# Optimization experiments

Hardware: AMD Instinct MI355X
Metric: run time of the kernel (lower is better)

The kernel has to match this reference:

```python
import jax, jax.numpy as jnp
import numpy as np

VOCAB, EMB, H, L, B, S = 100000, 300, 256, 2, 64, 512


def _lstm_cell(x, h, c, w_ih, w_hh, b_ih, b_hh):
    # PyTorch gate order: i, f, g, o
    g = x @ w_ih.T + h @ w_hh.T + (b_ih + b_hh)
    i, f, gg, o = jnp.split(g, 4, axis=-1)
    i, f, o = jax.nn.sigmoid(i), jax.nn.sigmoid(f), jax.nn.sigmoid(o)
    c_new = f * c + i * jnp.tanh(gg)
    h_new = o * jnp.tanh(c_new)
    return h_new, c_new


def setup_inputs() -> dict:
    key = jax.random.key(0)
    ks = jax.random.split(key, 16)
    k = 1.0 / np.sqrt(H)
    u = lambda kk, shape: jax.random.uniform(kk, shape, jnp.float32, -k, k)
    inp = {
        "contexts": jax.random.randint(ks[0], (B, S), 0, VOCAB),
        "positions": jax.random.randint(ks[1], (B,), 0, S),
        "emb": jax.random.normal(ks[2], (VOCAB, EMB), jnp.float32) * 0.1,
        # layer 0: input width EMB; layer 1: input width 2H. dim0 = direction (fwd, bwd)
        "w_ih_l0": u(ks[3], (2, 4 * H, EMB)),
        "w_hh_l0": u(ks[4], (2, 4 * H, H)),
        "b_ih_l0": u(ks[5], (2, 4 * H)),
        "b_hh_l0": u(ks[6], (2, 4 * H)),
        "w_ih_l1": u(ks[7], (2, 4 * H, 2 * H)),
        "w_hh_l1": u(ks[8], (2, 4 * H, H)),
        "b_ih_l1": u(ks[9], (2, 4 * H)),
        "b_hh_l1": u(ks[10], (2, 4 * H)),
        "w_cls": u(ks[11], (2, 2 * H)),
        "b_cls": u(ks[12], (2,)),
    }
    return inp


def reference(emb, w_ih_l0, w_hh_l0, b_ih_l0, b_hh_l0,
              w_ih_l1, w_hh_l1, b_ih_l1, b_hh_l1,
              w_cls, b_cls, contexts, positions):
    layers = [(w_ih_l0, w_hh_l0, b_ih_l0, b_hh_l0),
              (w_ih_l1, w_hh_l1, b_ih_l1, b_hh_l1)]
    bsz = contexts.shape[0]

    def step(carry, tok):
        h, c = carry  # (L, 2, B, H) each
        x = emb[tok]  # (B, EMB) — per-timestep embedding gather
        new_h, new_c = [], []
        for l, (wih, whh, bih, bhh) in enumerate(layers):
            outs = []
            # NOTE: original calls the bidirectional LSTM with seq_len=1 while
            # threading hidden state, so BOTH directions step forward in time.
            for d in range(2):
                hh, cc = _lstm_cell(x, h[l, d], c[l, d], wih[d], whh[d], bih[d], bhh[d])
                outs.append(hh); new_h.append(hh); new_c.append(cc)
            x = jnp.concatenate(outs, axis=-1)  # (B, 2H) -> input to next layer
        h = jnp.stack(new_h).reshape(len(layers), 2, bsz, H)
        c = jnp.stack(new_c).reshape(len(layers), 2, bsz, H)
        return (h, c), x

    h0 = jnp.zeros((len(layers), 2, bsz, H), jnp.float32)
    carry0 = (h0, h0)
    tokens = contexts.T  # (S, B): scan over sequence dim
    _, contexts_encoded = jax.lax.scan(step, carry0, tokens)  # (S, B, 2H)

    # gather encoded state at each item's target position
    target_output = contexts_encoded[positions, jnp.arange(bsz)]  # (B, 2H)
    logits = target_output @ w_cls.T + b_cls  # (B, 2)
    probs = jax.nn.sigmoid(logits)
    return (logits, probs, target_output)
```

## Files before the change

kernel.cpp:

```cpp
#include <hip/hip_runtime.h>
#include <hip/hip_cooperative_groups.h>


typedef short v8s __attribute__((ext_vector_type(8)));
typedef float v4f __attribute__((ext_vector_type(4)));
typedef unsigned long long u64;

#define S_LEN 512
#define BATCH 64
#define EMBD  300
#define XPAD  320
#define ROWP0 584
#define ROWP1 776

__device__ inline unsigned short f2bf(float x) {
  union { float f; unsigned u; } v; v.f = x;
  unsigned r = v.u + 0x7FFF + ((v.u >> 16) & 1);
  return (unsigned short)(r >> 16);
}
__device__ inline float sigm(float x) { return 1.f / (1.f + __expf(-x)); }
__device__ inline float tanhf_(float x) {
  float e = __expf(-2.f * fabsf(x));
  float r = (1.f - e) / (1.f + e);
  return x >= 0.f ? r : -r;
}

__device__ inline v8s ld_sys16(const unsigned short* p) {
  union { u64 q[2]; v8s s; } u;
  u.q[0] = __hip_atomic_load((const u64*)p,     __ATOMIC_RELAXED, __HIP_MEMORY_SCOPE_SYSTEM);
  u.q[1] = __hip_atomic_load((const u64*)p + 1, __ATOMIC_RELAXED, __HIP_MEMORY_SCOPE_SYSTEM);
  return u.s;
}
__device__ inline float ldf_sys(const float* p) {
  return __hip_atomic_load(p, __ATOMIC_RELAXED, __HIP_MEMORY_SCOPE_SYSTEM);
}
__device__ inline void st4_sys(unsigned* p, unsigned v) {
  __hip_atomic_store(p, v, __ATOMIC_RELAXED, __HIP_MEMORY_SCOPE_SYSTEM);
}
__device__ inline void stf_sys(float* p, float v) {
  __hip_atomic_store(p, v, __ATOMIC_RELAXED, __HIP_MEMORY_SCOPE_SYSTEM);
}

__device__ inline void wait_ge(unsigned* c, unsigned thr) {
  while (__hip_atomic_load(c, __ATOMIC_RELAXED, __HIP_MEMORY_SCOPE_AGENT) < thr)
    __builtin_amdgcn_s_sleep(1);
}
__device__ inline void arrive(unsigned* c) {
  __hip_atomic_fetch_add(c, 1u, __ATOMIC_RELAXED, __HIP_MEMORY_SCOPE_AGENT);
}

template<int NK1, int NK2, int P2OFF, bool C1, bool C2>
__device__ inline void step_mm(const unsigned short* __restrict__ aP1,
                               const unsigned short* __restrict__ aP2,
                               const unsigned short* lds_t0,
                               const unsigned short* lds_t1,
                               v4f& acc0, v4f& acc1) {
  v8s a[NK1 + NK2];
#pragma unroll
  for (int i = 0; i < NK1; ++i)
    a[i] = C1 ? ld_sys16(aP1 + i * 32) : *(const v8s*)(aP1 + i * 32);
#pragma unroll
  for (int i = 0; i < NK2; ++i)
    a[NK1 + i] = C2 ? ld_sys16(aP2 + i * 32) : *(const v8s*)(aP2 + i * 32);
#pragma unroll
  for (int i = 0; i < NK1; ++i) {
    v8s b0 = *(const v8s*)(lds_t0 + i * 32);
    v8s b1 = *(const v8s*)(lds_t1 + i * 32);
    acc0 = __builtin_amdgcn_mfma_f32_16x16x32_bf16(a[i], b0, acc0, 0, 0, 0);
    acc1 = __builtin_amdgcn_mfma_f32_16x16x32_bf16(a[i], b1, acc1, 0, 0, 0);
  }
#pragma unroll
  for (int i = 0; i < NK2; ++i) {
    v8s b0 = *(const v8s*)(lds_t0 + P2OFF + i * 32);
    v8s b1 = *(const v8s*)(lds_t1 + P2OFF + i * 32);
    acc0 = __builtin_amdgcn_mfma_f32_16x16x32_bf16(a[NK1 + i], b0, acc0, 0, 0, 0);
    acc1 = __builtin_amdgcn_mfma_f32_16x16x32_bf16(a[NK1 + i], b1, acc1, 0, 0, 0);
  }
}

__global__ void __launch_bounds__(128, 1)
ContextAwareModel_9655086481739_kernel(
    const int* __restrict__ contexts, const int* __restrict__ positions,
    const float* __restrict__ emb,
    const float* __restrict__ wih0, const float* __restrict__ whh0,
    const float* __restrict__ bih0, const float* __restrict__ bhh0,
    const float* __restrict__ wih1, const float* __restrict__ whh1,
    const float* __restrict__ bih1, const float* __restrict__ bhh1,
    const float* __restrict__ wcls, const float* __restrict__ bcls,
    float* __restrict__ out, unsigned char* __restrict__ ws)
{
  __shared__ unsigned short smem[32 * ROWP1];

  const int wg   = blockIdx.x;
  const int tid  = threadIdx.x;
  const int layer  = wg >> 7;
  const int d      = (wg >> 6) & 1;
  const int colblk = (wg >> 1) & 31;
  const int mhalf  = wg & 1;
  const int wv   = tid >> 6;
  const int lane = tid & 63;
  const int quad = lane >> 4;
  const int lc   = lane & 15;
  const int hc0  = colblk * 8;
  const int hc   = hc0 + (lc & 7);
  const int m0   = mhalf * 32 + wv * 16;
  const int r_base = m0 + quad * 4;

  unsigned short* Xbuf  = (unsigned short*)ws;
  unsigned short* h0buf = (unsigned short*)(ws + 20971520u);
  unsigned short* h1buf = (unsigned short*)(ws + 20971520u + 262144u);
  float*          tgt   = (float*)(ws + 20971520u + 262144u + 131072u);
  unsigned*       cnt   = (unsigned*)(ws + 20971520u + 262144u + 131072u + 131072u);

  const int ROWP = layer ? ROWP1 : ROWP0;

  {
    for (int i = wg * 128 + tid; i < 196608; i += 256 * 128) h0buf[i] = 0;
    if (wg == 0) { for (int i = tid; i < 512; i += 128) cnt[i] = 0; }
  }
  {
    int gw2 = wg * 2 + wv;
    for (int rl = 0; rl < 64; ++rl) {
      int rr = gw2 * 64 + rl;
      int t = rr >> 6, b = rr & 63;
      int tok = contexts[b * S_LEN + t];
      const float* erow = emb + (long)tok * EMBD;
#pragma unroll
      for (int i = 0; i < 5; ++i) {
        int kk = i * 64 + lane;
        float v = (kk < EMBD) ? erow[kk] : 0.f;
        if (kk < XPAD) Xbuf[rr * XPAD + kk] = f2bf(v);
      }
    }
  }
  {
    const float* wih = layer ? wih1 : wih0;
    const float* whh = layer ? whh1 : whh0;
    const int KI  = layer ? 512 : 300;
    const int KIp = layer ? 512 : 320;
    const int KT  = layer ? 768 : 576;
    int lr = tid >> 2, sub = tid & 3;
    int c = lr & 15, T = lr >> 4;
    int gate = T * 2 + (c >> 3);
    int j = gate * 256 + hc0 + (c & 7);
    const float* wri = wih + (long)(d * 1024 + j) * KI;
    const float* wrh = whh + (long)(d * 1024 + j) * 256;
    for (int kk = sub; kk < ROWP; kk += 4) {
      float v = 0.f;
      if (kk < KI) v = wri[kk];
      else if (kk >= KIp && kk < KT) v = wrh[kk - KIp];
      smem[lr * ROWP + kk] = f2bf(v);
    }
  }
  float bias0, bias1;
  {
    const float* bi = layer ? bih1 : bih0;
    const float* bh = layer ? bhh1 : bhh0;
    int j0 = ((lc >> 3) & 1) * 256 + hc;
    int j1 = (2 + ((lc >> 3) & 1)) * 256 + hc;
    bias0 = bi[d * 1024 + j0] + bh[d * 1024 + j0];
    bias1 = bi[d * 1024 + j1] + bh[d * 1024 + j1];
  }
  int pos[4];
#pragma unroll
  for (int j = 0; j < 4; ++j) pos[j] = positions[r_base + j];

  float cst[4] = {0.f, 0.f, 0.f, 0.f};

  const unsigned short* lds_t0 = smem + lc * ROWP + quad * 8;
  const unsigned short* lds_t1 = smem + (16 + lc) * ROWP + quad * 8;

  cooperative_groups::grid_group gg = cooperative_groups::this_grid();
  __syncthreads();
  gg.sync();

  const bool hi = (lc & 8) != 0;

  if (layer == 0) {
    unsigned* c_own = cnt + (0 + d * 2 + mhalf) * 64;
    unsigned* c_l1a = cnt + (4 + 0 + mhalf) * 64;
    unsigned* c_l1b = cnt + (4 + 2 + mhalf) * 64;
    for (int t = 0; t < S_LEN; ++t) {
      if (tid == 0) {
        if (t) wait_ge(c_own, 32u * t);
        if (t >= 4) {
          unsigned thr = 32u * (t - 3);
          wait_ge(c_l1a, thr); wait_ge(c_l1b, thr);
        }
      }
      __syncthreads();
      v4f acc0 = {bias0, bias0, bias0, bias0};
      v4f acc1 = {bias1, bias1, bias1, bias1};
      const unsigned short* aP1 = Xbuf + (t * BATCH + m0 + lc) * XPAD + quad * 8;
      const unsigned short* aP2 = h0buf + ((t + 3) & 3) * 32768 + (m0 + lc) * 512 + d * 256 + quad * 8;
      step_mm<10, 8, 320, false, true>(aP1, aP2, lds_t0, lds_t1, acc0, acc1);
#pragma unroll
      for (int j = 0; j < 4; ++j) {
        float a0 = acc0[j], a1 = acc1[j];
        float o0 = __shfl_xor(a0, 8);
        float o1 = __shfl_xor(a1, 8);
        float iv = hi ? o0 : a0;
        float fv = hi ? a0 : o0;
        float gv = hi ? o1 : a1;
        float ov = hi ? a1 : o1;
        float ii = sigm(iv), ff = sigm(fv), ggt = tanhf_(gv), oo = sigm(ov);
        float cn = ff * cst[j] + ii * ggt;
        cst[j] = cn;
        float hv = oo * tanhf_(cn);
        unsigned hb = f2bf(hv);
        unsigned ob = ((unsigned)__shfl_xor((int)hb, 1)) & 0xFFFFu;
        if (lc < 8 && !(lc & 1)) {
          unsigned word = hb | (ob << 16);
          st4_sys((unsigned*)&h0buf[(t & 3) * 32768 + (r_base + j) * 512 + d * 256 + hc], word);
        }
      }
      asm volatile("s_waitcnt vmcnt(0)" ::: "memory");
      __syncthreads();
      if (tid == 0) arrive(c_own);
    }
  } else {
    unsigned* c_own = cnt + (4 + d * 2 + mhalf) * 64;
    unsigned* c_h0a = cnt + (0 + 0 + mhalf) * 64;
    unsigned* c_h0b = cnt + (0 + 2 + mhalf) * 64;
    for (int t = 0; t < S_LEN; ++t) {
      if (tid == 0) {
        unsigned thr = 32u * (t + 1);
        wait_ge(c_h0a, thr); wait_ge(c_h0b, thr);
        if (t) wait_ge(c_own, 32u * t);
      }
      __syncthreads();
      v4f acc0 = {bias0, bias0, bias0, bias0};
      v4f acc1 = {bias1, bias1, bias1, bias1};
      const unsigned short* aP1 = h0buf + (t & 3) * 32768 + (m0 + lc) * 512 + quad * 8;
      const unsigned short* aP2 = h1buf + ((t + 1) & 1) * 32768 + d * 16384 + (m0 + lc) * 256 + quad * 8;
      step_mm<16, 8, 512, true, true>(aP1, aP2, lds_t0, lds_t1, acc0, acc1);
#pragma unroll
      for (int j = 0; j < 4; ++j) {
        float a0 = acc0[j], a1 = acc1[j];
        float o0 = __shfl_xor(a0, 8);
        float o1 = __shfl_xor(a1, 8);
        float iv = hi ? o0 : a0;
        float fv = hi ? a0 : o0;
        float gv = hi ? o1 : a1;
        float ov = hi ? a1 : o1;
        float ii = sigm(iv), ff = sigm(fv), ggt = tanhf_(gv), oo = sigm(ov);
        float cn = ff * cst[j] + ii * ggt;
        cst[j] = cn;
        float hv = oo * tanhf_(cn);
        unsigned hb = f2bf(hv);
        unsigned ob = ((unsigned)__shfl_xor((int)hb, 1)) & 0xFFFFu;
        int r = r_base + j;
        if (lc < 8 && !(lc & 1)) {
          unsigned word = hb | (ob << 16);
          st4_sys((unsigned*)&h1buf[(t & 1) * 32768 + d * 16384 + r * 256 + hc], word);
        }
        if (lc < 8 && pos[j] == t) stf_sys(&tgt[r * 512 + d * 256 + hc], hv);
      }
      asm volatile("s_waitcnt vmcnt(0)" ::: "memory");
      __syncthreads();
      if (tid == 0) arrive(c_own);
    }
  }

  if (tid == 0) {
#pragma unroll
    for (int g = 4; g < 8; ++g) wait_ge(cnt + g * 64, 32u * S_LEN);
  }
  __syncthreads();

  {
    for (int i = wg * 128 + tid; i < BATCH * 512; i += 256 * 128) out[256 + i] = ldf_sys(&tgt[i]);
    int gw = wg * 2 + wv;
    if (gw < 128) {
      int b = gw >> 1, cl = gw & 1;
      float s = 0.f;
#pragma unroll
      for (int i = 0; i < 8; ++i) {
        int j = i * 64 + lane;
        s += ldf_sys(&tgt[b * 512 + j]) * wcls[cl * 512 + j];
      }
      s += __shfl_xor(s, 32); s += __shfl_xor(s, 16); s += __shfl_xor(s, 8);
      s += __shfl_xor(s, 4);  s += __shfl_xor(s, 2);  s += __shfl_xor(s, 1);
      if (lane == 0) {
        float L = s + bcls[cl];
        out[b * 2 + cl] = L;
        out[128 + b * 2 + cl] = sigm(L);
      }
    }
  }
}

extern "C" void kernel_launch(void* const* d_in, const int* in_sizes, int n_in,
                              void* d_out, int out_size, void* d_ws, size_t ws_size,
                              hipStream_t stream) {
  (void)in_sizes; (void)n_in; (void)out_size; (void)ws_size;
  const int*   contexts  = (const int*)d_in[0];
  const int*   positions = (const int*)d_in[1];
  const float* emb   = (const float*)d_in[2];
  const float* wih0  = (const float*)d_in[3];
  const float* whh0  = (const float*)d_in[4];
  const float* bih0  = (const float*)d_in[5];
  const float* bhh0  = (const float*)d_in[6];
  const float* wih1  = (const float*)d_in[7];
  const float* whh1  = (const float*)d_in[8];
  const float* bih1  = (const float*)d_in[9];
  const float* bhh1  = (const float*)d_in[10];
  const float* wcls  = (const float*)d_in[11];
  const float* bcls  = (const float*)d_in[12];
  float* out = (float*)d_out;
  unsigned char* ws = (unsigned char*)d_ws;

  void* args[] = { &contexts, &positions, &emb,
                   &wih0, &whh0, &bih0, &bhh0,
                   &wih1, &whh1, &bih1, &bhh1,
                   &wcls, &bcls, &out, &ws };
  hipLaunchCooperativeKernel((const void*)ContextAwareModel_9655086481739_kernel,
                             dim3(256), dim3(128), args, 0, stream);
}
```

Baseline: 3.627 ms.

## Replace atomic counters with per-workgroup flags polled in parallel by wave lanes

Swaps the shared atomic-add counters for one padded flag per workgroup. Each workgroup stores its step number, and the lanes of its waves poll all producer flags in parallel, so tid 0 no longer spins on counters serially. Layer 0 also issues its embedding-input loads before the wait, so the memory latency overlaps the synchronisation. The cost is more polling traffic across many cache lines and more register pressure from the hoisted operand array.

```diff
diff --git a/kernel.cpp b/kernel.cpp
--- a/kernel.cpp
+++ b/kernel.cpp
@@ -12,6 +12,7 @@
 #define XPAD  320
 #define ROWP0 584
 #define ROWP1 776
+#define NWG   256
 
 __device__ inline unsigned short f2bf(float x) {
   union { float f; unsigned u; } v; v.f = x;
@@ -34,6 +35,9 @@
 __device__ inline float ldf_sys(const float* p) {
   return __hip_atomic_load(p, __ATOMIC_RELAXED, __HIP_MEMORY_SCOPE_SYSTEM);
 }
+__device__ inline unsigned ldu_sys(const unsigned* p) {
+  return __hip_atomic_load(p, __ATOMIC_RELAXED, __HIP_MEMORY_SCOPE_SYSTEM);
+}
 __device__ inline void st4_sys(unsigned* p, unsigned v) {
   __hip_atomic_store(p, v, __ATOMIC_RELAXED, __HIP_MEMORY_SCOPE_SYSTEM);
 }
@@ -41,40 +45,31 @@
   __hip_atomic_store(p, v, __ATOMIC_RELAXED, __HIP_MEMORY_SCOPE_SYSTEM);
 }
 
-__device__ inline void wait_ge(unsigned* c, unsigned thr) {
-  while (__hip_atomic_load(c, __ATOMIC_RELAXED, __HIP_MEMORY_SCOPE_AGENT) < thr)
+__device__ inline void wave_poll(const unsigned* pollp, unsigned thr) {
+  if (__all((pollp == nullptr) || (thr == 0u)) ) return;
+  for (;;) {
+    bool ok = (pollp == nullptr) || (thr == 0u) || (ldu_sys(pollp) >= thr);
+    if (__all(ok)) break;
     __builtin_amdgcn_s_sleep(1);
-}
-__device__ inline void arrive(unsigned* c) {
-  __hip_atomic_fetch_add(c, 1u, __ATOMIC_RELAXED, __HIP_MEMORY_SCOPE_AGENT);
-}
-
-template<int NK1, int NK2, int P2OFF, bool C1, bool C2>
-__device__ inline void step_mm(const unsigned short* __restrict__ aP1,
-                               const unsigned short* __restrict__ aP2,
-                               const unsigned short* lds_t0,
-                               const unsigned short* lds_t1,
-                               v4f& acc0, v4f& acc1) {
-  v8s a[NK1 + NK2];
-#pragma unroll
-  for (int i = 0; i < NK1; ++i)
-    a[i] = C1 ? ld_sys16(aP1 + i * 32) : *(const v8s*)(aP1 + i * 32);
-#pragma unroll
-  for (int i = 0; i < NK2; ++i)
-    a[NK1 + i] = C2 ? ld_sys16(aP2 + i * 32) : *(const v8s*)(aP2 + i * 32);
-#pragma unroll
-  for (int i = 0; i < NK1; ++i) {
-    v8s b0 = *(const v8s*)(lds_t0 + i * 32);
-    v8s b1 = *(const v8s*)(lds_t1 + i * 32);
+  }
+}
+
+template<int NKA, int NKB, int P2OFF>
+__device__ inline void mfma_dual(const v8s* a, const unsigned short* t0,
+                                 const unsigned short* t1, v4f& acc0, v4f& acc1) {
+#pragma unroll
+  for (int i = 0; i < NKA; ++i) {
+    v8s b0 = *(const v8s*)(t0 + i * 32);
+    v8s b1 = *(const v8s*)(t1 + i * 32);
     acc0 = __builtin_amdgcn_mfma_f32_16x16x32_bf16(a[i], b0, acc0, 0, 0, 0);
     acc1 = __builtin_amdgcn_mfma_f32_16x16x32_bf16(a[i], b1, acc1, 0, 0, 0);
   }
 #pragma unroll
-  for (int i = 0; i < NK2; ++i) {
-    v8s b0 = *(const v8s*)(lds_t0 + P2OFF + i * 32);
-    v8s b1 = *(const v8s*)(lds_t1 + P2OFF + i * 32);
-    acc0 = __builtin_amdgcn_mfma_f32_16x16x32_bf16(a[NK1 + i], b0, acc0, 0, 0, 0);
-    acc1 = __builtin_amdgcn_mfma_f32_16x16x32_bf16(a[NK1 + i], b1, acc1, 0, 0, 0);
+  for (int i = 0; i < NKB; ++i) {
+    v8s b0 = *(const v8s*)(t0 + P2OFF + i * 32);
+    v8s b1 = *(const v8s*)(t1 + P2OFF + i * 32);
+    acc0 = __builtin_amdgcn_mfma_f32_16x16x32_bf16(a[NKA + i], b0, acc0, 0, 0, 0);
+    acc1 = __builtin_amdgcn_mfma_f32_16x16x32_bf16(a[NKA + i], b1, acc1, 0, 0, 0);
   }
 }
 
@@ -105,18 +100,19 @@
   const int hc   = hc0 + (lc & 7);
   const int m0   = mhalf * 32 + wv * 16;
   const int r_base = m0 + quad * 4;
+  const int gid  = layer * 4 + d * 2 + mhalf;
 
   unsigned short* Xbuf  = (unsigned short*)ws;
   unsigned short* h0buf = (unsigned short*)(ws + 20971520u);
   unsigned short* h1buf = (unsigned short*)(ws + 20971520u + 262144u);
   float*          tgt   = (float*)(ws + 20971520u + 262144u + 131072u);
-  unsigned*       cnt   = (unsigned*)(ws + 20971520u + 262144u + 131072u + 131072u);
+  unsigned*       flags = (unsigned*)(ws + 20971520u + 262144u + 131072u + 131072u);
 
   const int ROWP = layer ? ROWP1 : ROWP0;
 
   {
-    for (int i = wg * 128 + tid; i < 196608; i += 256 * 128) h0buf[i] = 0;
-    if (wg == 0) { for (int i = tid; i < 512; i += 128) cnt[i] = 0; }
+    for (int i = wg * 128 + tid; i < 196608; i += NWG * 128) h0buf[i] = 0;
+    if (wg == 0) { for (int i = tid; i < 2048; i += 128) flags[i] = 0; }
   }
   {
     int gw2 = wg * 2 + wv;
@@ -164,36 +160,57 @@
   int pos[4];
 #pragma unroll
   for (int j = 0; j < 4; ++j) pos[j] = positions[r_base + j];
-
   float cst[4] = {0.f, 0.f, 0.f, 0.f};
-
   const unsigned short* lds_t0 = smem + lc * ROWP + quad * 8;
   const unsigned short* lds_t1 = smem + (16 + lc) * ROWP + quad * 8;
+  const bool hi = (lc & 8) != 0;
+
+  const unsigned* pollp = nullptr;
+  int pollcls = -1;
+  if (layer == 0) {
+    if (wv == 0) {
+      if (lane < 32) { pollp = flags + (gid * 32 + lane) * 8;            pollcls = 0; }
+      else           { pollp = flags + ((4 + mhalf) * 32 + lane - 32) * 8; pollcls = 1; }
+    } else {
+      if (lane < 32) { pollp = flags + ((6 + mhalf) * 32 + lane) * 8;     pollcls = 1; }
+    }
+  } else {
+    if (wv == 0) {
+      if (lane < 32) { pollp = flags + (gid * 32 + lane) * 8;            pollcls = 0; }
+      else           { pollp = flags + ((0 + mhalf) * 32 + lane - 32) * 8; pollcls = 1; }
+    } else {
+      if (lane < 32) { pollp = flags + ((2 + mhalf) * 32 + lane) * 8;     pollcls = 1; }
+    }
+  }
+  unsigned* myflag = flags + (gid * 32 + colblk) * 8;
 
   cooperative_groups::grid_group gg = cooperative_groups::this_grid();
   __syncthreads();
   gg.sync();
 
-  const bool hi = (lc & 8) != 0;
-
   if (layer == 0) {
-    unsigned* c_own = cnt + (0 + d * 2 + mhalf) * 64;
-    unsigned* c_l1a = cnt + (4 + 0 + mhalf) * 64;
-    unsigned* c_l1b = cnt + (4 + 2 + mhalf) * 64;
     for (int t = 0; t < S_LEN; ++t) {
-      if (tid == 0) {
-        if (t) wait_ge(c_own, 32u * t);
-        if (t >= 4) {
-          unsigned thr = 32u * (t - 3);
-          wait_ge(c_l1a, thr); wait_ge(c_l1b, thr);
-        }
+      v8s a[18];
+      {
+        const unsigned short* aP1 = Xbuf + (t * BATCH + m0 + lc) * XPAD + quad * 8;
+#pragma unroll
+        for (int i = 0; i < 10; ++i) a[i] = *(const v8s*)(aP1 + i * 32);
+      }
+      {
+        unsigned thr = 0;
+        if (pollcls == 0) thr = (unsigned)t;
+        else if (pollcls == 1) thr = (t >= 4) ? (unsigned)(t - 3) : 0u;
+        wave_poll(pollp, thr);
       }
       __syncthreads();
+      {
+        const unsigned short* aP2 = h0buf + ((t + 3) & 3) * 32768 + (m0 + lc) * 512 + d * 256 + quad * 8;
+#pragma unroll
+        for (int i = 0; i < 8; ++i) a[10 + i] = ld_sys16(aP2 + i * 32);
+      }
       v4f acc0 = {bias0, bias0, bias0, bias0};
       v4f acc1 = {bias1, bias1, bias1, bias1};
-      const unsigned short* aP1 = Xbuf + (t * BATCH + m0 + lc) * XPAD + quad * 8;
-      const unsigned short* aP2 = h0buf + ((t + 3) & 3) * 32768 + (m0 + lc) * 512 + d * 256 + quad * 8;
-      step_mm<10, 8, 320, false, true>(aP1, aP2, lds_t0, lds_t1, acc0, acc1);
+      mfma_dual<10, 8, 320>(a, lds_t0, lds_t1, acc0, acc1);
 #pragma unroll
       for (int j = 0; j < 4; ++j) {
         float a0 = acc0[j], a1 = acc1[j];
@@ -216,24 +233,30 @@
       }
       asm volatile("s_waitcnt vmcnt(0)" ::: "memory");
       __syncthreads();
-      if (tid == 0) arrive(c_own);
+      if (tid == 0) st4_sys(myflag, (unsigned)(t + 1));
     }
   } else {
-    unsigned* c_own = cnt + (4 + d * 2 + mhalf) * 64;
-    unsigned* c_h0a = cnt + (0 + 0 + mhalf) * 64;
-    unsigned* c_h0b = cnt + (0 + 2 + mhalf) * 64;
     for (int t = 0; t < S_LEN; ++t) {
-      if (tid == 0) {
-        unsigned thr = 32u * (t + 1);
-        wait_ge(c_h0a, thr); wait_ge(c_h0b, thr);
-        if (t) wait_ge(c_own, 32u * t);
+      {
+        unsigned thr = (pollcls == 0) ? (unsigned)t
+                     : (pollcls == 1) ? (unsigned)(t + 1) : 0u;
+        wave_poll(pollp, thr);
       }
       __syncthreads();
+      v8s a[24];
+      {
+        const unsigned short* p = h0buf + (t & 3) * 32768 + (m0 + lc) * 512 + quad * 8;
+#pragma unroll
+        for (int i = 0; i < 16; ++i) a[i] = ld_sys16(p + i * 32);
+      }
+      {
+        const unsigned short* p = h1buf + ((t + 1) & 1) * 32768 + d * 16384 + (m0 + lc) * 256 + quad * 8;
+#pragma unroll
+        for (int i = 0; i < 8; ++i) a[16 + i] = ld_sys16(p + i * 32);
+      }
       v4f acc0 = {bias0, bias0, bias0, bias0};
       v4f acc1 = {bias1, bias1, bias1, bias1};
-      const unsigned short* aP1 = h0buf + (t & 3) * 32768 + (m0 + lc) * 512 + quad * 8;
-      const unsigned short* aP2 = h1buf + ((t + 1) & 1) * 32768 + d * 16384 + (m0 + lc) * 256 + quad * 8;
-      step_mm<16, 8, 512, true, true>(aP1, aP2, lds_t0, lds_t1, acc0, acc1);
+      mfma_dual<16, 8, 512>(a, lds_t0, lds_t1, acc0, acc1);
 #pragma unroll
       for (int j = 0; j < 4; ++j) {
         float a0 = acc0[j], a1 = acc1[j];
@@ -258,33 +281,34 @@
       }
       asm volatile("s_waitcnt vmcnt(0)" ::: "memory");
       __syncthreads();
-      if (tid == 0) arrive(c_own);
-    }
-  }
-
-  if (tid == 0) {
-#pragma unroll
-    for (int g = 4; g < 8; ++g) wait_ge(cnt + g * 64, 32u * S_LEN);
+      if (tid == 0) st4_sys(myflag, (unsigned)(t + 1));
+    }
+  }
+
+  {
+    int g = (wv == 0) ? 4 : 6;
+    const unsigned* jp = flags + ((g + (lane >> 5)) * 32 + (lane & 31)) * 8;
+    wave_poll(jp, (unsigned)S_LEN);
   }
   __syncthreads();
 
   {
-    for (int i = wg * 128 + tid; i < BATCH * 512; i += 256 * 128) out[256 + i] = ldf_sys(&tgt[i]);
+    for (int i = wg * 128 + tid; i < BATCH * 512; i += NWG * 128) out[256 + i] = ldf_sys(&tgt[i]);
     int gw = wg * 2 + wv;
     if (gw < 128) {
-      int b = gw >> 1, cl = gw & 1;
+      int b = gw >> 1, cl2 = gw & 1;
       float s = 0.f;
 #pragma unroll
       for (int i = 0; i < 8; ++i) {
         int j = i * 64 + lane;
-        s += ldf_sys(&tgt[b * 512 + j]) * wcls[cl * 512 + j];
+        s += ldf_sys(&tgt[b * 512 + j]) * wcls[cl2 * 512 + j];
       }
       s += __shfl_xor(s, 32); s += __shfl_xor(s, 16); s += __shfl_xor(s, 8);
       s += __shfl_xor(s, 4);  s += __shfl_xor(s, 2);  s += __shfl_xor(s, 1);
       if (lane == 0) {
-        float L = s + bcls[cl];
-        out[b * 2 + cl] = L;
-        out[128 + b * 2 + cl] = sigm(L);
+        float L = s + bcls[cl2];
+        out[b * 2 + cl2] = L;
+        out[128 + b * 2 + cl2] = sigm(L);
       }
     }
   }
@@ -315,5 +339,5 @@
                    &wih1, &whh1, &bih1, &bhh1,
                    &wcls, &bcls, &out, &ws };
   hipLaunchCooperativeKernel((const void*)ContextAwareModel_9655086481739_kernel,
-                             dim3(256), dim3(128), args, 0, stream);
-}
+                             dim3(NWG), dim3(128), args, 0, stream);
+}
```

After: 3.069 ms. 1.18x faster.
